# Performance work log

Hardware: AMD Instinct MI355X
Metric: run time of the kernel (lower is better)

The kernel has to match this reference:

```python
import jax, jax.numpy as jnp
from jax import lax
import numpy as np

# sym6 reconstruction low-pass (pywt Wavelet('sym6').filter_bank[2]), length 12
SYM6_REC = [-0.007800708325034148, 0.0017677118642428036, 0.04472490177066578,
            -0.021060292512300564, -0.07263752278646252, 0.3379294217276218,
            0.787641141030194, 0.4910559419267466, -0.048311742585633,
            -0.11799011114819057, 0.0034907120842174702, 0.015404109327027373]

UP, DOWN = 1, 2
PAD = (len(SYM6_REC) - UP) // 2  # = 5


def setup_inputs() -> dict:
    key = jax.random.key(0)
    h = jnp.asarray(SYM6_REC, dtype=jnp.float32)
    kernel = h[None, :] * h[:, None]  # [12, 12] separable outer product
    x = jax.random.normal(key, (16, 64, 256, 256), dtype=jnp.float32)
    return {"input": x, "kernel": kernel}


def reference(input, kernel):
    # upfirdn2d: zero-insert upsample (lhs_dilation), pad, FIR convolve
    # (true convolution => flip kernel for lax correlation), strided downsample.
    B, C, H, W = input.shape
    w = jnp.flip(kernel, (0, 1))[None, None]        # [1, 1, kh, kw]
    x = input.reshape(B * C, 1, H, W)               # depthwise via batch fold
    y = lax.conv_general_dilated(
        x, w,
        window_strides=(DOWN, DOWN),
        padding=[(PAD, PAD), (PAD, PAD)],
        lhs_dilation=(UP, UP),
        dimension_numbers=('NCHW', 'OIHW', 'NCHW'))
    return y.reshape(B, C, y.shape[-2], y.shape[-1])
```

## Files before the change

### kernel.cpp

```cpp
#include <hip/hip_runtime.h>


#define H_IN  256
#define W_IN  256
#define H_OUT 128
#define W_OUT 128
#define KTAP  12
#define VSTR  276
#define FG    68
#define NTHR  256

typedef float f32x4 __attribute__((ext_vector_type(4)));

__global__ __launch_bounds__(NTHR)
void upfirdn2d_sym6(const float* __restrict__ x,
                    const float* __restrict__ k2d,
                    float* __restrict__ out) {
    __shared__ float vs[64 * VSTR];
    __shared__ float rsum[KTAP];

    const int tid = threadIdx.x;

    if (tid < KTAP) {
        const float4* kp = reinterpret_cast<const float4*>(k2d + 12 * tid);
        float4 a = kp[0], b = kp[1], c = kp[2];
        rsum[tid] = ((a.x + a.y) + (a.z + a.w))
                  + ((b.x + b.y) + (b.z + b.w))
                  + ((c.x + c.y) + (c.z + c.w));
    }
    __syncthreads();
    float w[KTAP];
    {
        float tot = 0.f;
        #pragma unroll
        for (int q = 0; q < KTAP; ++q) tot += rsum[q];
        const float r = rsqrtf(tot);
        #pragma unroll
        for (int p = 0; p < KTAP; ++p) w[p] = rsum[KTAP - 1 - p] * r;
    }

    const int bid = blockIdx.x;
    const int nb  = (bid & 7) * 256 + (bid >> 3);
    const int img = nb >> 1;
    const int ti  = nb & 1;

    const float* xim = x + (size_t)img * (H_IN * W_IN);
    float* oim = out + (size_t)img * (H_OUT * W_OUT);

    if (tid < 136) {
        const int sg  = tid / FG;
        const int cg  = tid - sg * FG;
        const int col = -8 + 4 * cg;
        const bool colok = (unsigned)col < (unsigned)W_IN;
        const int gr0 = 128 * ti + 64 * sg - 5;
        const int lr0 = 32 * sg;

        const float* rp = xim + (size_t)gr0 * W_IN + col;
        float4 sv[10];

        {
            float4 acc[16];
            #pragma unroll
            for (int k = 0; k < 16; ++k) acc[k] = make_float4(0.f, 0.f, 0.f, 0.f);

            #pragma unroll
            for (int rr = 0; rr < 42; ++rr) {
                const int gr = gr0 + rr;
                float4 v = make_float4(0.f, 0.f, 0.f, 0.f);
                if (colok && (unsigned)gr < (unsigned)H_IN)
                    v = *reinterpret_cast<const float4*>(rp);
                rp += W_IN;
                if (rr >= 32) sv[rr - 32] = v;
                #pragma unroll
                for (int ri = 0; ri < 16; ++ri) {
                    const int p = rr - 2 * ri;
                    if (p >= 0 && p < KTAP) {
                        acc[ri].x = fmaf(w[p], v.x, acc[ri].x);
                        acc[ri].y = fmaf(w[p], v.y, acc[ri].y);
                        acc[ri].z = fmaf(w[p], v.z, acc[ri].z);
                        acc[ri].w = fmaf(w[p], v.w, acc[ri].w);
                    }
                }
            }
            #pragma unroll
            for (int ri = 0; ri < 16; ++ri)
                *reinterpret_cast<float4*>(&vs[(lr0 + ri) * VSTR + 4 * cg]) = acc[ri];
        }

        {
            float4 acc[16];
            #pragma unroll
            for (int k = 0; k < 16; ++k) acc[k] = make_float4(0.f, 0.f, 0.f, 0.f);

            #pragma unroll
            for (int rr2 = 0; rr2 < 42; ++rr2) {
                const int gr = gr0 + 32 + rr2;
                float4 v;
                if (rr2 < 10) {
                    v = sv[rr2];
                } else {
                    v = make_float4(0.f, 0.f, 0.f, 0.f);
                    if (colok && (unsigned)gr < (unsigned)H_IN)
                        v = *reinterpret_cast<const float4*>(rp);
                    rp += W_IN;
                }
                #pragma unroll
                for (int ri = 0; ri < 16; ++ri) {
                    const int p = rr2 - 2 * ri;
                    if (p >= 0 && p < KTAP) {
                        acc[ri].x = fmaf(w[p], v.x, acc[ri].x);
                        acc[ri].y = fmaf(w[p], v.y, acc[ri].y);
                        acc[ri].z = fmaf(w[p], v.z, acc[ri].z);
                        acc[ri].w = fmaf(w[p], v.w, acc[ri].w);
                    }
                }
            }
            #pragma unroll
            for (int ri = 0; ri < 16; ++ri)
                *reinterpret_cast<float4*>(&vs[(lr0 + 16 + ri) * VSTR + 4 * cg]) = acc[ri];
        }
    }
    __syncthreads();

    for (int t = tid; t < 1024; t += NTHR) {
        const int i = t >> 4;
        const int g = t & 15;

        float f[32];
        #pragma unroll
        for (int m = 0; m < 8; ++m) {
            float4 v4 = *reinterpret_cast<const float4*>(&vs[i * VSTR + 16 * g + 4 * m]);
            f[4*m+0] = v4.x; f[4*m+1] = v4.y; f[4*m+2] = v4.z; f[4*m+3] = v4.w;
        }
        float o[8];
        #pragma unroll
        for (int jj = 0; jj < 8; ++jj) {
            float a = 0.f;
            #pragma unroll
            for (int q = 0; q < KTAP; ++q)
                a = fmaf(w[q], f[2*jj + 3 + q], a);
            o[jj] = a;
        }
        const int orow = 64 * ti + i;
        const int ocol = 8 * g;
        f32x4 o0 = { o[0], o[1], o[2], o[3] };
        f32x4 o1 = { o[4], o[5], o[6], o[7] };
        float* dst = oim + (size_t)orow * W_OUT + ocol;
        __builtin_nontemporal_store(o0, reinterpret_cast<f32x4*>(dst));
        __builtin_nontemporal_store(o1, reinterpret_cast<f32x4*>(dst + 4));
    }
}

extern "C" void kernel_launch(void* const* d_in, const int* in_sizes, int n_in,
                              void* d_out, int out_size, void* d_ws, size_t ws_size,
                              hipStream_t stream) {
    const float* x   = (const float*)d_in[0];
    const float* k2d = (const float*)d_in[1];
    float* out       = (float*)d_out;

    dim3 grid(2048);
    dim3 block(NTHR);
    upfirdn2d_sym6<<<grid, block, 0, stream>>>(x, k2d, out);
}
```

Before: 60.92 us.

## Halve shared vertical buffer by splitting passes into two phases with early stores

Splits the vertical and horizontal passes into two half-tile phases so the shared buffer only holds 32 rows instead of 64. Each accumulator row is written to shared memory as soon as its last tap is applied, instead of all rows being stored after the loop. Both changes aim to cut LDS use per block, letting more blocks sit on each CU, and to lower register pressure. The cost is two extra block-wide barriers and serialised phases: only 136 of 256 threads work during the vertical passes, and the other threads wait.

```diff
diff --git a/kernel.cpp b/kernel.cpp
--- a/kernel.cpp
+++ b/kernel.cpp
@@ -16,7 +16,7 @@
 void upfirdn2d_sym6(const float* __restrict__ x,
                     const float* __restrict__ k2d,
                     float* __restrict__ out) {
-    __shared__ float vs[64 * VSTR];
+    __shared__ float vs[32 * VSTR];
     __shared__ float rsum[KTAP];
 
     const int tid = threadIdx.x;
@@ -47,85 +47,49 @@
     const float* xim = x + (size_t)img * (H_IN * W_IN);
     float* oim = out + (size_t)img * (H_OUT * W_OUT);
 
-    if (tid < 136) {
-        const int sg  = tid / FG;
-        const int cg  = tid - sg * FG;
-        const int col = -8 + 4 * cg;
-        const bool colok = (unsigned)col < (unsigned)W_IN;
-        const int gr0 = 128 * ti + 64 * sg - 5;
-        const int lr0 = 32 * sg;
+    const int sg  = (tid < FG) ? 0 : 1;
+    const int cg  = tid - sg * FG;
+    const int col = -8 + 4 * cg;
+    const bool colok = (unsigned)col < (unsigned)W_IN;
+    const int gr0 = 128 * ti + 64 * sg - 5;
+    const bool vactive = (tid < 136);
 
-        const float* rp = xim + (size_t)gr0 * W_IN + col;
-        float4 sv[10];
+    const float* rp = xim + (size_t)gr0 * W_IN + col;
+    float* vrow = &vs[(size_t)(16 * sg) * VSTR + 4 * cg];
+    float4 sv[10];
 
-        {
-            float4 acc[16];
+    if (vactive) {
+        float4 acc[16];
+        #pragma unroll
+        for (int k = 0; k < 16; ++k) acc[k] = make_float4(0.f, 0.f, 0.f, 0.f);
+
+        #pragma unroll
+        for (int rr = 0; rr < 42; ++rr) {
+            const int gr = gr0 + rr;
+            float4 v = make_float4(0.f, 0.f, 0.f, 0.f);
+            if (colok && (unsigned)gr < (unsigned)H_IN)
+                v = *reinterpret_cast<const float4*>(rp);
+            rp += W_IN;
+            if (rr >= 32) sv[rr - 32] = v;
             #pragma unroll
-            for (int k = 0; k < 16; ++k) acc[k] = make_float4(0.f, 0.f, 0.f, 0.f);
-
-            #pragma unroll
-            for (int rr = 0; rr < 42; ++rr) {
-                const int gr = gr0 + rr;
-                float4 v = make_float4(0.f, 0.f, 0.f, 0.f);
-                if (colok && (unsigned)gr < (unsigned)H_IN)
-                    v = *reinterpret_cast<const float4*>(rp);
-                rp += W_IN;
-                if (rr >= 32) sv[rr - 32] = v;
-                #pragma unroll
-                for (int ri = 0; ri < 16; ++ri) {
-                    const int p = rr - 2 * ri;
-                    if (p >= 0 && p < KTAP) {
-                        acc[ri].x = fmaf(w[p], v.x, acc[ri].x);
-                        acc[ri].y = fmaf(w[p], v.y, acc[ri].y);
-                        acc[ri].z = fmaf(w[p], v.z, acc[ri].z);
-                        acc[ri].w = fmaf(w[p], v.w, acc[ri].w);
-                    }
+            for (int ri = 0; ri < 16; ++ri) {
+                const int p = rr - 2 * ri;
+                if (p >= 0 && p < KTAP) {
+                    acc[ri].x = fmaf(w[p], v.x, acc[ri].x);
+                    acc[ri].y = fmaf(w[p], v.y, acc[ri].y);
+                    acc[ri].z = fmaf(w[p], v.z, acc[ri].z);
+                    acc[ri].w = fmaf(w[p], v.w, acc[ri].w);
+                    if (p == KTAP - 1)
+                        *reinterpret_cast<float4*>(vrow + (size_t)ri * VSTR) = acc[ri];
                 }
             }
-            #pragma unroll
-            for (int ri = 0; ri < 16; ++ri)
-                *reinterpret_cast<float4*>(&vs[(lr0 + ri) * VSTR + 4 * cg]) = acc[ri];
-        }
-
-        {
-            float4 acc[16];
-            #pragma unroll
-            for (int k = 0; k < 16; ++k) acc[k] = make_float4(0.f, 0.f, 0.f, 0.f);
-
-            #pragma unroll
-            for (int rr2 = 0; rr2 < 42; ++rr2) {
-                const int gr = gr0 + 32 + rr2;
-                float4 v;
-                if (rr2 < 10) {
-                    v = sv[rr2];
-                } else {
-                    v = make_float4(0.f, 0.f, 0.f, 0.f);
-                    if (colok && (unsigned)gr < (unsigned)H_IN)
-                        v = *reinterpret_cast<const float4*>(rp);
-                    rp += W_IN;
-                }
-                #pragma unroll
-                for (int ri = 0; ri < 16; ++ri) {
-                    const int p = rr2 - 2 * ri;
-                    if (p >= 0 && p < KTAP) {
-                        acc[ri].x = fmaf(w[p], v.x, acc[ri].x);
-                        acc[ri].y = fmaf(w[p], v.y, acc[ri].y);
-                        acc[ri].z = fmaf(w[p], v.z, acc[ri].z);
-                        acc[ri].w = fmaf(w[p], v.w, acc[ri].w);
-                    }
-                }
-            }
-            #pragma unroll
-            for (int ri = 0; ri < 16; ++ri)
-                *reinterpret_cast<float4*>(&vs[(lr0 + 16 + ri) * VSTR + 4 * cg]) = acc[ri];
         }
     }
     __syncthreads();
 
-    for (int t = tid; t < 1024; t += NTHR) {
+    for (int t = tid; t < 512; t += NTHR) {
         const int i = t >> 4;
         const int g = t & 15;
-
         float f[32];
         #pragma unroll
         for (int m = 0; m < 8; ++m) {
@@ -141,7 +105,68 @@
                 a = fmaf(w[q], f[2*jj + 3 + q], a);
             o[jj] = a;
         }
-        const int orow = 64 * ti + i;
+        const int orow = 64 * ti + i + (i & 16);
+        const int ocol = 8 * g;
+        f32x4 o0 = { o[0], o[1], o[2], o[3] };
+        f32x4 o1 = { o[4], o[5], o[6], o[7] };
+        float* dst = oim + (size_t)orow * W_OUT + ocol;
+        __builtin_nontemporal_store(o0, reinterpret_cast<f32x4*>(dst));
+        __builtin_nontemporal_store(o1, reinterpret_cast<f32x4*>(dst + 4));
+    }
+    __syncthreads();
+
+    if (vactive) {
+        float4 acc[16];
+        #pragma unroll
+        for (int k = 0; k < 16; ++k) acc[k] = make_float4(0.f, 0.f, 0.f, 0.f);
+
+        #pragma unroll
+        for (int rr2 = 0; rr2 < 42; ++rr2) {
+            const int gr = gr0 + 32 + rr2;
+            float4 v;
+            if (rr2 < 10) {
+                v = sv[rr2];
+            } else {
+                v = make_float4(0.f, 0.f, 0.f, 0.f);
+                if (colok && (unsigned)gr < (unsigned)H_IN)
+                    v = *reinterpret_cast<const float4*>(rp);
+                rp += W_IN;
+            }
+            #pragma unroll
+            for (int ri = 0; ri < 16; ++ri) {
+                const int p = rr2 - 2 * ri;
+                if (p >= 0 && p < KTAP) {
+                    acc[ri].x = fmaf(w[p], v.x, acc[ri].x);
+                    acc[ri].y = fmaf(w[p], v.y, acc[ri].y);
+                    acc[ri].z = fmaf(w[p], v.z, acc[ri].z);
+                    acc[ri].w = fmaf(w[p], v.w, acc[ri].w);
+                    if (p == KTAP - 1)
+                        *reinterpret_cast<float4*>(vrow + (size_t)ri * VSTR) = acc[ri];
+                }
+            }
+        }
+    }
+    __syncthreads();
+
+    for (int t = tid; t < 512; t += NTHR) {
+        const int i = t >> 4;
+        const int g = t & 15;
+        float f[32];
+        #pragma unroll
+        for (int m = 0; m < 8; ++m) {
+            float4 v4 = *reinterpret_cast<const float4*>(&vs[i * VSTR + 16 * g + 4 * m]);
+            f[4*m+0] = v4.x; f[4*m+1] = v4.y; f[4*m+2] = v4.z; f[4*m+3] = v4.w;
+        }
+        float o[8];
+        #pragma unroll
+        for (int jj = 0; jj < 8; ++jj) {
+            float a = 0.f;
+            #pragma unroll
+            for (int q = 0; q < KTAP; ++q)
+                a = fmaf(w[q], f[2*jj + 3 + q], a);
+            o[jj] = a;
+        }
+        const int orow = 64 * ti + i + (i & 16) + 16;
         const int ocol = 8 * g;
         f32x4 o0 = { o[0], o[1], o[2], o[3] };
         f32x4 o1 = { o[4], o[5], o[6], o[7] };
```

Result: slower. 70.61 us (+15.9%).
